# Kernel tuning notes

Measured on AMD Instinct MI355X. Metric: run time of the kernel, lower is better.

The kernel has to match this reference:

```python
import jax, jax.numpy as jnp
import numpy as np

B, H, T, K, V = 2, 8, 2048, 128, 128


def setup_inputs() -> dict:
    key = jax.random.key(0)
    k1, k2, k3, k4, k5 = jax.random.split(key, 5)
    return {
        "q": jax.random.normal(k1, (B, H, T, K), dtype=jnp.float32),
        "k": jax.random.normal(k2, (B, H, T, K), dtype=jnp.float32),
        "v": jax.random.normal(k3, (B, H, T, V), dtype=jnp.float32),
        "i_gate": jax.random.normal(k4, (B, H, T), dtype=jnp.float32),
        "f_gate": jax.random.normal(k5, (B, H, T), dtype=jnp.float32),
    }


def reference(q, k, v, i_gate, f_gate):
    # Stabilized parallel mLSTM (same math as the chunked Triton kernel,
    # expressed in natural-log base instead of base-2).
    Bq, Hq, Tq, Kd = q.shape
    scale = Kd ** -0.5
    logf = jax.nn.log_sigmoid(f_gate)                      # [B,H,T]
    fc = jnp.cumsum(logf, axis=-1)                         # cumulative forget logits
    # log decay matrix: logD[t,s] = i[s] + (fc[t] - fc[s]) for s <= t
    logD = fc[..., :, None] - fc[..., None, :] + i_gate[..., None, :]  # [B,H,T,T]
    mask = jnp.tril(jnp.ones((Tq, Tq), dtype=bool))
    logD_masked = jnp.where(mask, logD, -jnp.inf)
    m = jnp.max(logD_masked, axis=-1)                      # row-wise stabilizer [B,H,T]
    D = jnp.where(mask, jnp.exp(logD - m[..., None]), 0.0) # stabilized decay matrix
    S = jnp.einsum("bhtk,bhsk->bhts", q, k) * scale * D    # gated scores
    norm = jnp.maximum(jnp.abs(jnp.sum(S, axis=-1)), jnp.exp(-m))  # [B,H,T]
    h = jnp.einsum("bhts,bhsv->bhtv", S, v) / norm[..., None]
    return h
```

## Files before the change

### kernel.cpp

```cpp
#include <hip/hip_runtime.h>

#define T_SEQ 2048
#define DHEAD 128
#define NBH 16
#define SCALE 0.08838834764831845f

typedef unsigned short u16;
typedef unsigned int u32;
typedef u16 u16x4 __attribute__((ext_vector_type(4)));
typedef u16 u16x8 __attribute__((ext_vector_type(8)));
typedef u32 u32x2 __attribute__((ext_vector_type(2)));
typedef short s16x4 __attribute__((ext_vector_type(4)));
typedef __bf16 bf16x8 __attribute__((ext_vector_type(8)));
typedef float f32x4 __attribute__((ext_vector_type(4)));

__device__ __forceinline__ u16 f2bfu(float x) {
  union { float f; unsigned u; } c; c.f = x;
  unsigned u = c.u;
  u = u + 0x7FFFu + ((u >> 16) & 1u);
  return (u16)(u >> 16);
}

__device__ __forceinline__ bf16x8 ldsFrag(const u16* p) {
  u16x8 t = *(const u16x8*)p;
  return __builtin_bit_cast(bf16x8, t);
}

__device__ __forceinline__ f32x4 mfma16x16x16bf16(s16x4 a, s16x4 b, f32x4 c) {
#if __has_builtin(__builtin_amdgcn_mfma_f32_16x16x16bf16_1k)
  return __builtin_amdgcn_mfma_f32_16x16x16bf16_1k(a, b, c, 0, 0, 0);
#else
  asm("v_mfma_f32_16x16x16_bf16 %0, %1, %2, %0" : "+v"(c) : "v"(a), "v"(b));
  return c;
#endif
}

__device__ __forceinline__ void gld_lds16(const void* g, void* l) {
  __builtin_amdgcn_global_load_lds(
      (__attribute__((address_space(1))) const unsigned int*)g,
      (__attribute__((address_space(3))) unsigned int*)l, 16, 0, 0);
}

__global__ __launch_bounds__(1024) void gate_scan_kernel(
    const float* __restrict__ ig, const float* __restrict__ fg,
    float* __restrict__ a_out, float* __restrict__ c_out,
    float* __restrict__ fc_out)
{
  const int bh = blockIdx.x, tid = threadIdx.x;
  const int w = tid >> 6, lane = tid & 63;
  const int base = bh * T_SEQ + tid * 2;
  __shared__ float wsum[16];
  __shared__ float wmax[16];

  const float x0 = fg[base], x1 = fg[base + 1];
  const float ls0 = fminf(x0, 0.f) - log1pf(expf(-fabsf(x0)));
  const float ls1 = fminf(x1, 0.f) - log1pf(expf(-fabsf(x1)));
  const float s = ls0 + ls1;

  float sc = s;
#pragma unroll
  for (int off = 1; off < 64; off <<= 1) {
    const float t = __shfl_up(sc, off, 64);
    if (lane >= off) sc += t;
  }
  if (lane == 63) wsum[w] = sc;
  __syncthreads();
  float wo = 0.f;
#pragma unroll
  for (int i = 0; i < 15; ++i) if (i < w) wo += wsum[i];
  const float excl = wo + (sc - s);
  const float fc0 = excl + ls0;
  const float fc1 = excl + ls0 + ls1;
  fc_out[base] = fc0; fc_out[base + 1] = fc1;
  const float a0 = ig[base] - fc0;
  const float a1 = ig[base + 1] - fc1;
  a_out[base] = a0; a_out[base + 1] = a1;

  const float m = fmaxf(a0, a1);
  float mc = m;
#pragma unroll
  for (int off = 1; off < 64; off <<= 1) {
    const float t = __shfl_up(mc, off, 64);
    if (lane >= off) mc = fmaxf(mc, t);
  }
  if (lane == 63) wmax[w] = mc;
  __syncthreads();
  float wmo = -INFINITY;
#pragma unroll
  for (int i = 0; i < 15; ++i) if (i < w) wmo = fmaxf(wmo, wmax[i]);
  const float prev = __shfl_up(mc, 1, 64);
  float exclm = (lane > 0) ? prev : -INFINITY;
  exclm = fmaxf(exclm, wmo);
  c_out[base] = fmaxf(exclm, a0);
  c_out[base + 1] = fmaxf(exclm, m);
}

__global__ __launch_bounds__(256) void cvt_kv_kernel(
    const float* __restrict__ kk, const float* __restrict__ v,
    const float* __restrict__ ag, const float* __restrict__ cg,
    u16* __restrict__ kbf, u16* __restrict__ vt)
{
  const int bh = blockIdx.y, kt = blockIdx.x, tid = threadIdx.x;
  {
    const int r = tid >> 2;
    const int c0 = (tid & 3) * 32;
    const int row = kt * 64 + r;
    const float sc = __expf(ag[bh * T_SEQ + row] - cg[bh * T_SEQ + (row | 63)]);
    const float* sp = kk + ((size_t)bh * T_SEQ + row) * DHEAD + c0;
    u16* dp = kbf + ((size_t)bh * T_SEQ + row) * DHEAD + c0;
#pragma unroll
    for (int j = 0; j < 8; ++j) {
      const float4 x = *(const float4*)(sp + j * 4);
      u16x4 pq;
      pq[0] = f2bfu(x.x * sc); pq[1] = f2bfu(x.y * sc);
      pq[2] = f2bfu(x.z * sc); pq[3] = f2bfu(x.w * sc);
      *(u16x4*)(dp + j * 4) = pq;
    }
  }
  __shared__ __align__(16) u16 L[128 * 72];
  const int n0 = (tid & 31) * 4, k0 = (tid >> 5) * 8;
  const float* vp = v + ((size_t)bh * T_SEQ + kt * 64 + k0) * DHEAD + n0;
  u16 tv[4][8];
#pragma unroll
  for (int rr = 0; rr < 8; ++rr) {
    const float4 x = *(const float4*)(vp + rr * DHEAD);
    tv[0][rr] = f2bfu(x.x); tv[1][rr] = f2bfu(x.y);
    tv[2][rr] = f2bfu(x.z); tv[3][rr] = f2bfu(x.w);
  }
#pragma unroll
  for (int j = 0; j < 4; ++j) {
    u16x8 pq;
#pragma unroll
    for (int rr = 0; rr < 8; ++rr) pq[rr] = tv[j][rr];
    *(u16x8*)(&L[(n0 + j) * 72 + k0]) = pq;
  }
  __syncthreads();
  const int row = tid >> 1, s0 = (tid & 1) * 32;
  u16* op = vt + ((size_t)bh * DHEAD + row) * T_SEQ + kt * 64 + s0;
#pragma unroll
  for (int i = 0; i < 4; ++i)
    *(u16x8*)(op + i * 8) = *(const u16x8*)(&L[row * 72 + s0 + i * 8]);
}

template <bool FAST>
__global__ __launch_bounds__(1024, 4) void mlstm_fwd_kernel(
    const float* __restrict__ qg, const float* __restrict__ kxg,
    const float* __restrict__ vg,
    const u16* __restrict__ kbf, const u16* __restrict__ vtbf,
    const float* __restrict__ ag, const float* __restrict__ cg,
    const float* __restrict__ fcg, float* __restrict__ out)
{
  const int bx = (int)blockIdx.x;
  const int bh = bx & 15, p = bx >> 4;
  const int tid = (int)threadIdx.x;
  const int w = tid >> 6, lane = tid & 63;
  const int quad = lane >> 4, l16 = lane & 15;
  const int kg = w & 3, rq = w >> 2;

  const int qtA = 31 - p, qtB = p;
  const int nA = qtA + 1, nB = qtB + 1;

  __shared__ __align__(16) unsigned char SM[148992];
  u16* Kst = (u16*)SM;
  float* osh = (float*)(SM + 131072);
  float* rsh = (float*)(SM + 147968);

  const size_t hoff = (size_t)bh * T_SEQ * DHEAD;
  const int goff = bh * T_SEQ;

  bf16x8 qf[4];
  auto loadQ = [&](int lqt) {
    const float* qp = qg + hoff + (size_t)(lqt * 64 + rq * 16 + l16) * DHEAD + quad * 8;
#pragma unroll
    for (int kc = 0; kc < 4; ++kc) {
      const float4 x0 = *(const float4*)(qp + kc * 32);
      const float4 x1 = *(const float4*)(qp + kc * 32 + 4);
      u16x8 t;
      t[0] = f2bfu(x0.x); t[1] = f2bfu(x0.y); t[2] = f2bfu(x0.z); t[3] = f2bfu(x0.w);
      t[4] = f2bfu(x1.x); t[5] = f2bfu(x1.y); t[6] = f2bfu(x1.z); t[7] = f2bfu(x1.w);
      qf[kc] = __builtin_bit_cast(bf16x8, t);
    }
  };

  f32x4 oa[8];
  float rsacc;
  auto zeroAcc = [&]() {
#pragma unroll
    for (int mt = 0; mt < 8; ++mt) oa[mt] = (f32x4){0.f, 0.f, 0.f, 0.f};
    rsacc = 0.f;
  };
  zeroAcc();

  const int skey = tid >> 4, sdb = (tid & 15) ^ (skey & 7);
  const u16* ksBase = kbf + (size_t)goff * DHEAD + (size_t)skey * DHEAD + sdb * 8;
  const int svn = tid >> 3, svk = (tid & 7) ^ (svn & 7);
  const u16* vsBase = vtbf + (size_t)bh * DHEAD * T_SEQ + (size_t)svn * T_SEQ + svk * 8;

  auto stage = [&](int st, int slot) {
    u16* KbL = Kst + slot * 16384;
    u16* VbL = Kst + slot * 16384 + 8192;
    if (FAST) {
      gld_lds16(ksBase + (size_t)st * 64 * DHEAD, KbL + w * 512);
      gld_lds16(vsBase + st * 64, VbL + w * 512);
    } else {
      const float ct = cg[goff + st * 64 + 63];
      const float* kp = kxg + hoff + (size_t)(st * 64) * DHEAD;
      const float* vp = vg + hoff + (size_t)(st * 64) * DHEAD;
      { const float scv = __expf(ag[goff + st * 64 + skey] - ct);
        const float4 x0 = *(const float4*)(kp + (size_t)skey * DHEAD + sdb * 8);
        const float4 x1 = *(const float4*)(kp + (size_t)skey * DHEAD + sdb * 8 + 4);
        u16x8 pk;
        pk[0] = f2bfu(x0.x * scv); pk[1] = f2bfu(x0.y * scv);
        pk[2] = f2bfu(x0.z * scv); pk[3] = f2bfu(x0.w * scv);
        pk[4] = f2bfu(x1.x * scv); pk[5] = f2bfu(x1.y * scv);
        pk[6] = f2bfu(x1.z * scv); pk[7] = f2bfu(x1.w * scv);
        *(u16x8*)(KbL + tid * 8) = pk; }
      { u16x8 pw;
#pragma unroll
        for (int rr = 0; rr < 8; ++rr)
          pw[rr] = f2bfu(vp[(size_t)(svk * 8 + rr) * DHEAD + svn]);
        *(u16x8*)(VbL + tid * 8) = pw; }
    }
  };
  auto stagePair = [&](int s0, int lim, int pr) {
    if (s0 < lim)     stage(s0,     pr * 2);
    if (s0 + 1 < lim) stage(s0 + 1, pr * 2 + 1);
  };

  const int keyA = kg * 16 + l16;
  const int ksw  = l16 & 7;
  const int kbu  = kg * 2 + (quad >> 1);
  const int vbase = l16 * 64 + ((kbu ^ (l16 & 7)) * 8) + (quad & 1) * 4;

  auto computeStage = [&](int cqt, int st, int slot, float ccmax) {
    const u16* KbL = Kst + slot * 16384;
    const u16* VbL = Kst + slot * 16384 + 8192;

    f32x4 sa = (f32x4){0.f, 0.f, 0.f, 0.f};
#pragma unroll
    for (int kc = 0; kc < 4; ++kc) {
      const bf16x8 kf = ldsFrag(KbL + keyA * 128 + (((kc * 4 + quad) ^ ksw) * 8));
      sa = __builtin_amdgcn_mfma_f32_16x16x32_bf16(kf, qf[kc], sa, 0, 0, 0);
    }

    const float etile = SCALE * __expf(cg[goff + st * 64 + 63] - ccmax);
    float x0 = sa[0] * etile, x1 = sa[1] * etile;
    float x2 = sa[2] * etile, x3 = sa[3] * etile;
    if (st == cqt) {
      const int qr = rq * 16 + l16, kb0 = kg * 16 + quad * 4;
      if (kb0 + 0 > qr) x0 = 0.f;
      if (kb0 + 1 > qr) x1 = 0.f;
      if (kb0 + 2 > qr) x2 = 0.f;
      if (kb0 + 3 > qr) x3 = 0.f;
    }
    rsacc += (x0 + x1) + (x2 + x3);
    u32 plo, phi;
    asm("v_cvt_pk_bf16_f32 %0, %1, %2" : "=v"(plo) : "v"(x0), "v"(x1));
    asm("v_cvt_pk_bf16_f32 %0, %1, %2" : "=v"(phi) : "v"(x2), "v"(x3));
    const s16x4 pfr = __builtin_bit_cast(s16x4, (u32x2){plo, phi});

#pragma unroll
    for (int mt = 0; mt < 8; ++mt) {
      const s16x4 va = *(const s16x4*)(VbL + vbase + mt * 1024);
      oa[mt] = mfma16x16x16bf16(va, pfr, oa[mt]);
    }
  };

  auto epilogue = [&](int eqt, float ecmax) {
    float x = rsacc;
    x += __shfl_xor(x, 16, 64);
    x += __shfl_xor(x, 32, 64);
    if (lane < 16) rsh[kg * 64 + rq * 16 + lane] = x;
    __syncthreads();
    float inv = 0.f;
    if (kg == 3) {
      const int row = rq * 16 + l16;
      const float tot = rsh[row] + rsh[64 + row] + rsh[128 + row] + rsh[192 + row];
      const float nf = __expf(-(ecmax + fcg[goff + eqt * 64 + row]));
      inv = 1.f / fmaxf(fabsf(tot), nf);
    }
    const int srow = tid >> 4, scol = tid & 15;
#pragma unroll
    for (int h = 0; h < 2; ++h) {
      for (int r = 0; r < 4; ++r) {
        if (kg == r) {
          const int row = rq * 16 + l16;
#pragma unroll
          for (int ml = 0; ml < 4; ++ml) {
            float* ap = osh + row * 66 + ml * 16 + quad * 4;
            f32x4 vv = oa[h * 4 + ml];
            if (r > 0) vv = vv + *(const f32x4*)ap;
            if (r == 3) vv = vv * inv;
            *(f32x4*)ap = vv;
          }
        }
        __syncthreads();
      }
      {
        const f32x4 vv = *(const f32x4*)(osh + srow * 66 + scol * 4);
        *(f32x4*)(out + hoff + (size_t)(eqt * 64 + srow) * DHEAD + h * 64 + scol * 4) = vv;
      }
      __syncthreads();
    }
  };

  int qt = qtA, n = nA;
  float cmax = cg[goff + qtA * 64 + 63];
  loadQ(qtA);
  stagePair(0, nA, 0);
  __syncthreads();

  int pr = 0;
  for (int phase = 0; phase < 2; ++phase) {
    const int c = (n + 1) >> 1;
    for (int g = 0; g < c; ++g) {
      if (g + 1 < c)        stagePair(2 * (g + 1), n, pr ^ 1);
      else if (phase == 0)  stagePair(0, nB, pr ^ 1);
      computeStage(qt, 2 * g, pr * 2, cmax);
      if (2 * g + 1 < n) computeStage(qt, 2 * g + 1, pr * 2 + 1, cmax);
      __syncthreads();
      pr ^= 1;
    }
    if (phase == 0) loadQ(qtB);
    epilogue(qt, cmax);
    if (phase == 0) {
      zeroAcc();
      qt = qtB; n = nB;
      cmax = cg[goff + qtB * 64 + 63];
    }
  }
}

extern "C" void kernel_launch(void* const* d_in, const int* in_sizes, int n_in,
                              void* d_out, int out_size, void* d_ws, size_t ws_size,
                              hipStream_t stream) {
  const float* q  = (const float*)d_in[0];
  const float* k  = (const float*)d_in[1];
  const float* v  = (const float*)d_in[2];
  const float* ig = (const float*)d_in[3];
  const float* fg = (const float*)d_in[4];

  const size_t gate_bytes = (size_t)3 * NBH * T_SEQ * sizeof(float);
  const size_t kv_elems   = (size_t)NBH * T_SEQ * DHEAD;
  const bool fast = ws_size >= gate_bytes + 2 * kv_elems * sizeof(u16);

  float* a_ws  = (float*)d_ws;
  float* c_ws  = a_ws + NBH * T_SEQ;
  float* fc_ws = c_ws + NBH * T_SEQ;
  u16* kbf  = (u16*)((char*)d_ws + gate_bytes);
  u16* vtbf = kbf + kv_elems;

  gate_scan_kernel<<<dim3(NBH), dim3(1024), 0, stream>>>(ig, fg, a_ws, c_ws, fc_ws);
  if (fast) {
    cvt_kv_kernel<<<dim3(T_SEQ / 64, NBH), dim3(256), 0, stream>>>(
        k, v, a_ws, c_ws, kbf, vtbf);
    mlstm_fwd_kernel<true><<<dim3(256), dim3(1024), 0, stream>>>(
        q, k, v, kbf, vtbf, a_ws, c_ws, fc_ws, (float*)d_out);
  } else {
    mlstm_fwd_kernel<false><<<dim3(256), dim3(1024), 0, stream>>>(
        q, k, v, kbf, vtbf, a_ws, c_ws, fc_ws, (float*)d_out);
  }
}
```

Measured before the change: 154.9 us.

## Halve block to 512 threads with each wave covering all 64 query rows

Result: slower. 326.6 us (+110.8%).

```diff
diff --git a/kernel.cpp b/kernel.cpp
--- a/kernel.cpp
+++ b/kernel.cpp
@@ -143,7 +143,7 @@
 }
 
 template <bool FAST>
-__global__ __launch_bounds__(1024, 4) void mlstm_fwd_kernel(
+__global__ __launch_bounds__(512, 1) void mlstm_fwd_kernel(
     const float* __restrict__ qg, const float* __restrict__ kxg,
     const float* __restrict__ vg,
     const u16* __restrict__ kbf, const u16* __restrict__ vtbf,
@@ -151,179 +151,225 @@
     const float* __restrict__ fcg, float* __restrict__ out)
 {
   const int bx = (int)blockIdx.x;
-  const int bh = bx & 15, p = bx >> 4;
+  const int bh = ((bx & 7) << 1) | ((bx >> 3) & 1);
+  const int p  = bx >> 4;
   const int tid = (int)threadIdx.x;
   const int w = tid >> 6, lane = tid & 63;
   const int quad = lane >> 4, l16 = lane & 15;
-  const int kg = w & 3, rq = w >> 2;
+  const int kg = w & 3, sg = w >> 2;
 
   const int qtA = 31 - p, qtB = p;
   const int nA = qtA + 1, nB = qtB + 1;
 
-  __shared__ __align__(16) unsigned char SM[148992];
+  __shared__ __align__(16) unsigned char SM[131072];
   u16* Kst = (u16*)SM;
-  float* osh = (float*)(SM + 131072);
-  float* rsh = (float*)(SM + 147968);
 
   const size_t hoff = (size_t)bh * T_SEQ * DHEAD;
   const int goff = bh * T_SEQ;
 
-  bf16x8 qf[4];
+  bf16x8 qf[16];
   auto loadQ = [&](int lqt) {
-    const float* qp = qg + hoff + (size_t)(lqt * 64 + rq * 16 + l16) * DHEAD + quad * 8;
-#pragma unroll
-    for (int kc = 0; kc < 4; ++kc) {
-      const float4 x0 = *(const float4*)(qp + kc * 32);
-      const float4 x1 = *(const float4*)(qp + kc * 32 + 4);
-      u16x8 t;
-      t[0] = f2bfu(x0.x); t[1] = f2bfu(x0.y); t[2] = f2bfu(x0.z); t[3] = f2bfu(x0.w);
-      t[4] = f2bfu(x1.x); t[5] = f2bfu(x1.y); t[6] = f2bfu(x1.z); t[7] = f2bfu(x1.w);
-      qf[kc] = __builtin_bit_cast(bf16x8, t);
+    const float* qp = qg + hoff + (size_t)(lqt * 64) * DHEAD;
+#pragma unroll
+    for (int nt = 0; nt < 4; ++nt) {
+      const float* qr = qp + (size_t)(nt * 16 + l16) * DHEAD + quad * 8;
+#pragma unroll
+      for (int kc = 0; kc < 4; ++kc) {
+        const float4 x0 = *(const float4*)(qr + kc * 32);
+        const float4 x1 = *(const float4*)(qr + kc * 32 + 4);
+        u16x8 t;
+        t[0] = f2bfu(x0.x); t[1] = f2bfu(x0.y); t[2] = f2bfu(x0.z); t[3] = f2bfu(x0.w);
+        t[4] = f2bfu(x1.x); t[5] = f2bfu(x1.y); t[6] = f2bfu(x1.z); t[7] = f2bfu(x1.w);
+        qf[nt * 4 + kc] = __builtin_bit_cast(bf16x8, t);
+      }
     }
   };
 
-  f32x4 oa[8];
-  float rsacc;
+  f32x4 oa[8][4];
+  float rsacc[4];
   auto zeroAcc = [&]() {
 #pragma unroll
-    for (int mt = 0; mt < 8; ++mt) oa[mt] = (f32x4){0.f, 0.f, 0.f, 0.f};
-    rsacc = 0.f;
+    for (int mt = 0; mt < 8; ++mt)
+#pragma unroll
+      for (int nt = 0; nt < 4; ++nt) oa[mt][nt] = (f32x4){0.f, 0.f, 0.f, 0.f};
+#pragma unroll
+    for (int nt = 0; nt < 4; ++nt) rsacc[nt] = 0.f;
   };
   zeroAcc();
 
-  const int skey = tid >> 4, sdb = (tid & 15) ^ (skey & 7);
-  const u16* ksBase = kbf + (size_t)goff * DHEAD + (size_t)skey * DHEAD + sdb * 8;
-  const int svn = tid >> 3, svk = (tid & 7) ^ (svn & 7);
-  const u16* vsBase = vtbf + (size_t)bh * DHEAD * T_SEQ + (size_t)svn * T_SEQ + svk * 8;
+  const int B0 = tid, B1 = tid + 512;
+  const int k0key = B0 >> 4, k0db = (B0 & 15) ^ (k0key & 7);
+  const int k1key = B1 >> 4, k1db = (B1 & 15) ^ (k1key & 7);
+  const int v0n = B0 >> 3, v0k = (B0 & 7) ^ (v0n & 7);
+  const int v1n = B1 >> 3, v1k = (B1 & 7) ^ (v1n & 7);
+  const u16* kG = kbf + (size_t)goff * DHEAD;
+  const u16* vG = vtbf + (size_t)bh * DHEAD * T_SEQ;
 
   auto stage = [&](int st, int slot) {
     u16* KbL = Kst + slot * 16384;
-    u16* VbL = Kst + slot * 16384 + 8192;
+    u16* VbL = KbL + 8192;
     if (FAST) {
-      gld_lds16(ksBase + (size_t)st * 64 * DHEAD, KbL + w * 512);
-      gld_lds16(vsBase + st * 64, VbL + w * 512);
+      const u16* ks = kG + (size_t)st * (64 * DHEAD);
+      const u16* vs = vG + st * 64;
+      gld_lds16(ks + k0key * DHEAD + k0db * 8, KbL + w * 512);
+      gld_lds16(ks + k1key * DHEAD + k1db * 8, KbL + 4096 + w * 512);
+      gld_lds16(vs + (size_t)v0n * T_SEQ + v0k * 8, VbL + w * 512);
+      gld_lds16(vs + (size_t)v1n * T_SEQ + v1k * 8, VbL + 4096 + w * 512);
     } else {
       const float ct = cg[goff + st * 64 + 63];
       const float* kp = kxg + hoff + (size_t)(st * 64) * DHEAD;
       const float* vp = vg + hoff + (size_t)(st * 64) * DHEAD;
-      { const float scv = __expf(ag[goff + st * 64 + skey] - ct);
-        const float4 x0 = *(const float4*)(kp + (size_t)skey * DHEAD + sdb * 8);
-        const float4 x1 = *(const float4*)(kp + (size_t)skey * DHEAD + sdb * 8 + 4);
+#pragma unroll
+      for (int j = 0; j < 2; ++j) {
+        const int key = j ? k1key : k0key, db = j ? k1db : k0db;
+        const int Bc = j ? B1 : B0;
+        const float scv = __expf(ag[goff + st * 64 + key] - ct);
+        const float4 x0 = *(const float4*)(kp + (size_t)key * DHEAD + db * 8);
+        const float4 x1 = *(const float4*)(kp + (size_t)key * DHEAD + db * 8 + 4);
         u16x8 pk;
         pk[0] = f2bfu(x0.x * scv); pk[1] = f2bfu(x0.y * scv);
         pk[2] = f2bfu(x0.z * scv); pk[3] = f2bfu(x0.w * scv);
         pk[4] = f2bfu(x1.x * scv); pk[5] = f2bfu(x1.y * scv);
         pk[6] = f2bfu(x1.z * scv); pk[7] = f2bfu(x1.w * scv);
-        *(u16x8*)(KbL + tid * 8) = pk; }
-      { u16x8 pw;
+        *(u16x8*)(KbL + Bc * 8) = pk;
+        const int n = j ? v1n : v0n, kb = j ? v1k : v0k;
+        u16x8 pw;
 #pragma unroll
         for (int rr = 0; rr < 8; ++rr)
-          pw[rr] = f2bfu(vp[(size_t)(svk * 8 + rr) * DHEAD + svn]);
-        *(u16x8*)(VbL + tid * 8) = pw; }
-    }
-  };
-  auto stagePair = [&](int s0, int lim, int pr) {
-    if (s0 < lim)     stage(s0,     pr * 2);
-    if (s0 + 1 < lim) stage(s0 + 1, pr * 2 + 1);
+          pw[rr] = f2bfu(vp[(size_t)(kb * 8 + rr) * DHEAD + n]);
+        *(u16x8*)(VbL + Bc * 8) = pw;
+      }
+    }
   };
 
   const int keyA = kg * 16 + l16;
   const int ksw  = l16 & 7;
-  const int kbu  = kg * 2 + (quad >> 1);
-  const int vbase = l16 * 64 + ((kbu ^ (l16 & 7)) * 8) + (quad & 1) * 4;
+  const int vbase = l16 * 64 + (((kg * 2 + (quad >> 1)) ^ (l16 & 7)) * 8) + (quad & 1) * 4;
 
   auto computeStage = [&](int cqt, int st, int slot, float ccmax) {
     const u16* KbL = Kst + slot * 16384;
-    const u16* VbL = Kst + slot * 16384 + 8192;
-
-    f32x4 sa = (f32x4){0.f, 0.f, 0.f, 0.f};
+    const u16* VbL = KbL + 8192;
+
+    f32x4 sa[4];
+#pragma unroll
+    for (int nt = 0; nt < 4; ++nt) sa[nt] = (f32x4){0.f, 0.f, 0.f, 0.f};
 #pragma unroll
     for (int kc = 0; kc < 4; ++kc) {
       const bf16x8 kf = ldsFrag(KbL + keyA * 128 + (((kc * 4 + quad) ^ ksw) * 8));
-      sa = __builtin_amdgcn_mfma_f32_16x16x32_bf16(kf, qf[kc], sa, 0, 0, 0);
+      sa[0] = __builtin_amdgcn_mfma_f32_16x16x32_bf16(kf, qf[0 * 4 + kc], sa[0], 0, 0, 0);
+      sa[1] = __builtin_amdgcn_mfma_f32_16x16x32_bf16(kf, qf[1 * 4 + kc], sa[1], 0, 0, 0);
+      sa[2] = __builtin_amdgcn_mfma_f32_16x16x32_bf16(kf, qf[2 * 4 + kc], sa[2], 0, 0, 0);
+      sa[3] = __builtin_amdgcn_mfma_f32_16x16x32_bf16(kf, qf[3 * 4 + kc], sa[3], 0, 0, 0);
     }
 
     const float etile = SCALE * __expf(cg[goff + st * 64 + 63] - ccmax);
-    float x0 = sa[0] * etile, x1 = sa[1] * etile;
-    float x2 = sa[2] * etile, x3 = sa[3] * etile;
-    if (st == cqt) {
-      const int qr = rq * 16 + l16, kb0 = kg * 16 + quad * 4;
-      if (kb0 + 0 > qr) x0 = 0.f;
-      if (kb0 + 1 > qr) x1 = 0.f;
-      if (kb0 + 2 > qr) x2 = 0.f;
-      if (kb0 + 3 > qr) x3 = 0.f;
-    }
-    rsacc += (x0 + x1) + (x2 + x3);
-    u32 plo, phi;
-    asm("v_cvt_pk_bf16_f32 %0, %1, %2" : "=v"(plo) : "v"(x0), "v"(x1));
-    asm("v_cvt_pk_bf16_f32 %0, %1, %2" : "=v"(phi) : "v"(x2), "v"(x3));
-    const s16x4 pfr = __builtin_bit_cast(s16x4, (u32x2){plo, phi});
+    const bool diag = (st == cqt);
+    const int kb0 = kg * 16 + quad * 4;
+
+    s16x4 pfr[4];
+#pragma unroll
+    for (int nt = 0; nt < 4; ++nt) {
+      float x0 = sa[nt][0] * etile, x1 = sa[nt][1] * etile;
+      float x2 = sa[nt][2] * etile, x3 = sa[nt][3] * etile;
+      if (diag) {
+        const int qr = nt * 16 + l16;
+        if (kb0 + 0 > qr) x0 = 0.f;
+        if (kb0 + 1 > qr) x1 = 0.f;
+        if (kb0 + 2 > qr) x2 = 0.f;
+        if (kb0 + 3 > qr) x3 = 0.f;
+      }
+      rsacc[nt] += (x0 + x1) + (x2 + x3);
+      u32 plo, phi;
+      asm("v_cvt_pk_bf16_f32 %0, %1, %2" : "=v"(plo) : "v"(x0), "v"(x1));
+      asm("v_cvt_pk_bf16_f32 %0, %1, %2" : "=v"(phi) : "v"(x2), "v"(x3));
+      pfr[nt] = __builtin_bit_cast(s16x4, (u32x2){plo, phi});
+    }
 
 #pragma unroll
     for (int mt = 0; mt < 8; ++mt) {
       const s16x4 va = *(const s16x4*)(VbL + vbase + mt * 1024);
-      oa[mt] = mfma16x16x16bf16(va, pfr, oa[mt]);
+      oa[mt][0] = mfma16x16x16bf16(va, pfr[0], oa[mt][0]);
+      oa[mt][1] = mfma16x16x16bf16(va, pfr[1], oa[mt][1]);
+      oa[mt][2] = mfma16x16x16bf16(va, pfr[2], oa[mt][2]);
+      oa[mt][3] = mfma16x16x16bf16(va, pfr[3], oa[mt][3]);
     }
   };
 
-  auto epilogue = [&](int eqt, float ecmax) {
-    float x = rsacc;
-    x += __shfl_xor(x, 16, 64);
-    x += __shfl_xor(x, 32, 64);
-    if (lane < 16) rsh[kg * 64 + rq * 16 + lane] = x;
+  auto epilogue = [&](int eqt, float ecmax, int dead) {
+    float* osh = (float*)(SM + dead * 65536);
+    float* rsh = osh + 64 * 132;
+    float* ish = rsh + 512;
+    float rst[4];
+#pragma unroll
+    for (int nt = 0; nt < 4; ++nt) {
+      float x = rsacc[nt];
+      x += __shfl_xor(x, 16, 64);
+      x += __shfl_xor(x, 32, 64);
+      rst[nt] = x;
+    }
+    if (lane < 16) {
+#pragma unroll
+      for (int nt = 0; nt < 4; ++nt) rsh[w * 64 + nt * 16 + lane] = rst[nt];
+    }
     __syncthreads();
-    float inv = 0.f;
-    if (kg == 3) {
-      const int row = rq * 16 + l16;
-      const float tot = rsh[row] + rsh[64 + row] + rsh[128 + row] + rsh[192 + row];
+    if (w == 7) {
+      const int row = lane;
+      float tot = 0.f;
+#pragma unroll
+      for (int j = 0; j < 8; ++j) tot += rsh[j * 64 + row];
       const float nf = __expf(-(ecmax + fcg[goff + eqt * 64 + row]));
-      inv = 1.f / fmaxf(fabsf(tot), nf);
-    }
-    const int srow = tid >> 4, scol = tid & 15;
-#pragma unroll
-    for (int h = 0; h < 2; ++h) {
-      for (int r = 0; r < 4; ++r) {
-        if (kg == r) {
-          const int row = rq * 16 + l16;
-#pragma unroll
-          for (int ml = 0; ml < 4; ++ml) {
-            float* ap = osh + row * 66 + ml * 16 + quad * 4;
-            f32x4 vv = oa[h * 4 + ml];
-            if (r > 0) vv = vv + *(const f32x4*)ap;
-            if (r == 3) vv = vv * inv;
-            *(f32x4*)ap = vv;
-          }
-        }
-        __syncthreads();
-      }
-      {
-        const f32x4 vv = *(const f32x4*)(osh + srow * 66 + scol * 4);
-        *(f32x4*)(out + hoff + (size_t)(eqt * 64 + srow) * DHEAD + h * 64 + scol * 4) = vv;
+      ish[row] = 1.f / fmaxf(fabsf(tot), nf);
+    }
+    __syncthreads();
+    for (int j = 0; j < 8; ++j) {
+      const int e = (w + j) & 7;
+#pragma unroll
+      for (int nt = 0; nt < 4; ++nt) {
+        float* ap = osh + (nt * 16 + l16) * 132 + e * 16 + quad * 4;
+        f32x4 vv = oa[e][nt];
+        if (j > 0) vv = vv + *(const f32x4*)ap;
+        if (j == 7) vv = vv * ish[nt * 16 + l16];
+        *(f32x4*)ap = vv;
       }
       __syncthreads();
     }
+    const int row = tid >> 3, c0 = (tid & 7) * 16;
+#pragma unroll
+    for (int i = 0; i < 4; ++i) {
+      const f32x4 vv = *(const f32x4*)(osh + row * 132 + c0 + i * 4);
+      *(f32x4*)(out + hoff + (size_t)(eqt * 64 + row) * DHEAD + c0 + i * 4) = vv;
+    }
+    __syncthreads();
   };
 
   int qt = qtA, n = nA;
   float cmax = cg[goff + qtA * 64 + 63];
   loadQ(qtA);
-  stagePair(0, nA, 0);
+  stage(0, 0);
+  stage(1, 1);
   __syncthreads();
 
   int pr = 0;
-  for (int phase = 0; phase < 2; ++phase) {
+  for (int ph = 0; ph < 2; ++ph) {
     const int c = (n + 1) >> 1;
     for (int g = 0; g < c; ++g) {
-      if (g + 1 < c)        stagePair(2 * (g + 1), n, pr ^ 1);
-      else if (phase == 0)  stagePair(0, nB, pr ^ 1);
-      computeStage(qt, 2 * g, pr * 2, cmax);
-      if (2 * g + 1 < n) computeStage(qt, 2 * g + 1, pr * 2 + 1, cmax);
+      if (g + 1 < c) {
+        const int s0 = 2 * (g + 1);
+        stage(s0, (pr ^ 1) * 2);
+        stage((s0 + 1 < n) ? s0 + 1 : s0, (pr ^ 1) * 2 + 1);
+      } else if (ph == 0) {
+        stage(0, (pr ^ 1) * 2);
+        stage((nB > 1) ? 1 : 0, (pr ^ 1) * 2 + 1);
+      }
+      const int st = 2 * g + sg;
+      if (st < n) computeStage(qt, st, pr * 2 + sg, cmax);
       __syncthreads();
       pr ^= 1;
     }
-    if (phase == 0) loadQ(qtB);
-    epilogue(qt, cmax);
-    if (phase == 0) {
+    const int dead = pr ^ 1;
+    if (ph == 0) loadQ(qtB);
+    epilogue(qt, cmax, dead);
+    if (ph == 0) {
       zeroAcc();
       qt = qtB; n = nB;
       cmax = cg[goff + qtB * 64 + 63];
@@ -354,10 +400,10 @@
   if (fast) {
     cvt_kv_kernel<<<dim3(T_SEQ / 64, NBH), dim3(256), 0, stream>>>(
         k, v, a_ws, c_ws, kbf, vtbf);
-    mlstm_fwd_kernel<true><<<dim3(256), dim3(1024), 0, stream>>>(
+    mlstm_fwd_kernel<true><<<dim3(256), dim3(512), 0, stream>>>(
         q, k, v, kbf, vtbf, a_ws, c_ws, fc_ws, (float*)d_out);
   } else {
-    mlstm_fwd_kernel<false><<<dim3(256), dim3(1024), 0, stream>>>(
+    mlstm_fwd_kernel<false><<<dim3(256), dim3(512), 0, stream>>>(
         q, k, v, kbf, vtbf, a_ws, c_ws, fc_ws, (float*)d_out);
   }
 }
```
